# Kernel tuning notes

Measured on AMD Instinct MI355X. Metric: run time of the kernel, lower is better.

## Reference

```python
import jax, jax.numpy as jnp
import numpy as np

B, T, D = 8, 1024, 1024
H, G = 16, 4            # num_heads, query_groups
HD = D // H             # head_dim = 64
REP = H // G            # heads_per_group
EPS = 1e-10
NEG = -1e9


def setup_inputs() -> dict:
    key = jax.random.key(0)
    k1, k2, k3 = jax.random.split(key, 3)
    x = jax.random.normal(k1, (B, T, D), dtype=jnp.float32)
    w_qkv = jax.random.normal(k2, (D, H * HD + 2 * G * HD), dtype=jnp.float32) * (D ** -0.5)
    w_o = jax.random.normal(k3, (D, D), dtype=jnp.float32) * (D ** -0.5)
    padding_mask = jnp.ones((B, T), dtype=bool)
    return {"x": x, "w_qkv": w_qkv, "w_o": w_o, "padding_mask": padding_mask}


def _l2_norm(t):
    # qk_norm_type=2: L2 normalize over head_dim
    return t / (jnp.sqrt(jnp.sum(t * t, axis=-1, keepdims=True)) + EPS)


def reference(x, w_qkv, w_o, padding_mask):
    # fused QKV projection: [B,T,D] @ [D, H*HD + 2*G*HD]
    qkv = x @ w_qkv
    q, k, v = jnp.split(qkv, [H * HD, H * HD + G * HD], axis=-1)
    q = q.reshape(B, T, H, HD)
    k = k.reshape(B, T, G, HD)
    v = v.reshape(B, T, G, HD)
    # QK normalization (L2 over head_dim)
    q = _l2_norm(q)
    k = _l2_norm(k)
    # GQA: expand KV heads (repeat_interleave along head dim)
    k = jnp.repeat(k, REP, axis=2)  # [B,T,H,HD]
    v = jnp.repeat(v, REP, axis=2)
    # to [B,H,T,HD]
    q = q.transpose(0, 2, 1, 3)
    k = k.transpose(0, 2, 1, 3)
    v = v.transpose(0, 2, 1, 3)
    # causal + padding mask, True = attend
    causal = jnp.tril(jnp.ones((T, T), dtype=bool))  # [T_q, T_k]
    valid = padding_mask[:, None, :, None] & padding_mask[:, None, None, :] & causal[None, None]
    scale = HD ** -0.5  # SDPA default scale
    scores = jnp.einsum('bhqd,bhkd->bhqk', q, k) * scale
    scores = jnp.where(valid, scores, NEG)
    attn = jax.nn.softmax(scores, axis=-1)
    out = jnp.einsum('bhqk,bhkd->bhqd', attn, v)  # [B,H,T,HD]
    out = out.transpose(0, 2, 1, 3).reshape(B, T, D)
    return out @ w_o
```

## Files before the change

### kernel.cpp

```cpp
#include <hip/hip_runtime.h>
#include <hip/hip_bf16.h>

typedef __attribute__((ext_vector_type(8))) short short8;
typedef __attribute__((ext_vector_type(4))) short short4v;
typedef __attribute__((ext_vector_type(4))) float f32x4;

#define B_ 8
#define T_ 1024
#define D_ 1024
#define H_ 16
#define G_ 4
#define HD_ 64
#define QKVW 1536

#define GLOAD16(gp, lp) __builtin_amdgcn_global_load_lds( \
    (const __attribute__((address_space(1))) void*)(gp),  \
    (__attribute__((address_space(3))) void*)(lp), 16, 0, 0)

__device__ __forceinline__ float exp2_fast(float x) {
    return __builtin_amdgcn_exp2f(x);
}

__device__ __forceinline__ short8 pack_bf16x8(float4 a, float4 b) {
    union { short8 s; __hip_bfloat16 h[8]; } u;
    u.h[0] = __float2bfloat16(a.x); u.h[1] = __float2bfloat16(a.y);
    u.h[2] = __float2bfloat16(a.z); u.h[3] = __float2bfloat16(a.w);
    u.h[4] = __float2bfloat16(b.x); u.h[5] = __float2bfloat16(b.y);
    u.h[6] = __float2bfloat16(b.z); u.h[7] = __float2bfloat16(b.w);
    return u.s;
}

__global__ __launch_bounds__(256) void cvt_transpose(
    const float* __restrict__ in, __hip_bfloat16* __restrict__ outT, int K, int N)
{
    __shared__ float tile[32][33];
    const int k0 = blockIdx.y * 32, n0 = blockIdx.x * 32;
    const int r = threadIdx.x >> 5, c = threadIdx.x & 31;
    #pragma unroll
    for (int i = 0; i < 4; ++i)
        tile[r + i * 8][c] = in[(size_t)(k0 + r + i * 8) * N + n0 + c];
    __syncthreads();
    #pragma unroll
    for (int i = 0; i < 4; ++i)
        outT[(size_t)(n0 + r + i * 8) * K + k0 + c] = __float2bfloat16(tile[c][r + i * 8]);
}

__global__ __launch_bounds__(256) void gemm_qkv(
    const float* __restrict__ Af,
    const __hip_bfloat16* __restrict__ Bt,
    __hip_bfloat16* __restrict__ qkv,
    __hip_bfloat16* __restrict__ vt)
{
    const int M = B_ * T_, K = D_;
    __shared__ __hip_bfloat16 As[2][128 * 32];
    __shared__ __hip_bfloat16 Bs[2][128 * 32];

    const int tid  = threadIdx.x;
    const int lane = tid & 63;
    const int wr   = (tid >> 6) >> 1;
    const int wc   = (tid >> 6) & 1;

    const int rpx = (M >> 7) >> 3;
    const int xcd = blockIdx.x & 7;
    const int lin = blockIdx.x >> 3;
    const int by  = xcd * rpx + (lin % rpx);
    const int bx  = lin / rpx;
    const int m0 = by * 128;
    const int n0 = bx * 128;

    f32x4 acc[4][4] = {};

    const int sr0 = tid >> 2;
    const int sr1 = 64 + sr0;
    const int slot  = (tid & 3) ^ ((tid >> 3) & 3);
    const int sc_ln = (tid & 3) * 8;
    const int sc_sw = slot * 8;
    const int ws0 = sr0 * 64 + slot * 16;
    const int ws1 = sr1 * 64 + slot * 16;

    const float* Ar0f = Af + (size_t)(m0 + sr0) * K + sc_ln;
    const float* Ar1f = Af + (size_t)(m0 + sr1) * K + sc_ln;
    const __hip_bfloat16* Br0 = Bt + (size_t)(n0 + sr0) * K + sc_sw;
    const __hip_bfloat16* Br1 = Bt + (size_t)(n0 + sr1) * K + sc_sw;

    const int fr = lane & 15;
    const int kb = (lane >> 4) * 16;
    const int swzg = ((fr >> 1) & 3) << 4;

    float4 a0a = *(const float4*)(Ar0f);
    float4 a0b = *(const float4*)(Ar0f + 4);
    float4 a1a = *(const float4*)(Ar1f);
    float4 a1b = *(const float4*)(Ar1f + 4);
    GLOAD16(Br0, (char*)&Bs[0][0] + tid * 16);
    GLOAD16(Br1, (char*)&Bs[0][0] + 4096 + tid * 16);
    *(short8*)((char*)&As[0][0] + ws0) = pack_bf16x8(a0a, a0b);
    *(short8*)((char*)&As[0][0] + ws1) = pack_bf16x8(a1a, a1b);
    __syncthreads();

    int cur = 0;
    for (int kk = 0; kk < K; kk += 32) {
        const int nxt = cur ^ 1;
        const bool more = (kk + 32 < K);
        if (more) {
            a0a = *(const float4*)(Ar0f + kk + 32);
            a0b = *(const float4*)(Ar0f + kk + 36);
            a1a = *(const float4*)(Ar1f + kk + 32);
            a1b = *(const float4*)(Ar1f + kk + 36);
            GLOAD16(Br0 + kk + 32, (char*)&Bs[nxt][0] + tid * 16);
            GLOAD16(Br1 + kk + 32, (char*)&Bs[nxt][0] + 4096 + tid * 16);
        }
        short8 a[4], b[4];
        #pragma unroll
        for (int m = 0; m < 4; ++m)
            a[m] = *(const short8*)((char*)&As[cur][0] +
                    (wr * 64 + m * 16 + fr) * 64 + (kb ^ swzg));
        #pragma unroll
        for (int n = 0; n < 4; ++n)
            b[n] = *(const short8*)((char*)&Bs[cur][0] +
                    (wc * 64 + n * 16 + fr) * 64 + (kb ^ swzg));
        #pragma unroll
        for (int m = 0; m < 4; ++m)
            #pragma unroll
            for (int n = 0; n < 4; ++n)
                acc[m][n] = __builtin_amdgcn_mfma_f32_16x16x32_bf16(a[m], b[n], acc[m][n], 0, 0, 0);
        if (more) {
            *(short8*)((char*)&As[nxt][0] + ws0) = pack_bf16x8(a0a, a0b);
            *(short8*)((char*)&As[nxt][0] + ws1) = pack_bf16x8(a1a, a1b);
        }
        __syncthreads();
        cur = nxt;
    }

    const int rowb  = m0 + wr * 64 + (lane >> 4) * 4;
    const int colb0 = n0 + wc * 64;

    if (n0 < 1280) {
        const float extra = (n0 < 1024) ? 0.18033688f : 1.0f;
        #pragma unroll
        for (int m = 0; m < 4; ++m)
            #pragma unroll
            for (int r = 0; r < 4; ++r) {
                float ss = 0.f;
                #pragma unroll
                for (int n = 0; n < 4; ++n) { float v = acc[m][n][r]; ss += v * v; }
                ss += __shfl_xor(ss, 1, 64);
                ss += __shfl_xor(ss, 2, 64);
                ss += __shfl_xor(ss, 4, 64);
                ss += __shfl_xor(ss, 8, 64);
                float sc = extra / (sqrtf(ss) + 1e-10f);
                const size_t rbase = (size_t)(rowb + m * 16 + r) * QKVW + colb0 + fr;
                #pragma unroll
                for (int n = 0; n < 4; ++n)
                    qkv[rbase + n * 16] = __float2bfloat16(acc[m][n][r] * sc);
            }
    } else {
        #pragma unroll
        for (int m = 0; m < 4; ++m) {
            const int row = rowb + m * 16;
            const int bb  = row >> 10;
            const int t0  = row & 1023;
            #pragma unroll
            for (int n = 0; n < 4; ++n) {
                const int cv = colb0 + fr + n * 16 - 1280;
                const int gg = cv >> 6, d = cv & 63;
                union { short4v s; __hip_bfloat16 h[4]; } u;
                u.h[0] = __float2bfloat16(acc[m][n][0]);
                u.h[1] = __float2bfloat16(acc[m][n][1]);
                u.h[2] = __float2bfloat16(acc[m][n][2]);
                u.h[3] = __float2bfloat16(acc[m][n][3]);
                *reinterpret_cast<short4v*>(
                    vt + ((size_t)((bb * G_ + gg) * HD_ + d)) * T_ + t0) = u.s;
            }
        }
    }
}

__global__ __launch_bounds__(256) void gemm_tn_f32(
    const __hip_bfloat16* __restrict__ A,
    const __hip_bfloat16* __restrict__ Bt,
    float* __restrict__ C, int M, int N, int K)
{
    __shared__ __hip_bfloat16 As[2][128 * 32];
    __shared__ __hip_bfloat16 Bs[2][128 * 32];

    const int tid  = threadIdx.x;
    const int lane = tid & 63;
    const int wr   = (tid >> 6) >> 1;
    const int wc   = (tid >> 6) & 1;

    const int rpx = (M >> 7) >> 3;
    const int xcd = blockIdx.x & 7;
    const int lin = blockIdx.x >> 3;
    const int by  = xcd * rpx + (lin % rpx);
    const int bx  = lin / rpx;
    const int m0 = by * 128;
    const int n0 = bx * 128;

    f32x4 acc[4][4] = {};

    const int sr0 = tid >> 2;
    const int sr1 = 64 + sr0;
    const int slot  = (tid & 3) ^ ((tid >> 3) & 3);
    const int sc_sw = slot * 8;

    const __hip_bfloat16* Ar0 = A  + (size_t)(m0 + sr0) * K + sc_sw;
    const __hip_bfloat16* Ar1 = A  + (size_t)(m0 + sr1) * K + sc_sw;
    const __hip_bfloat16* Br0 = Bt + (size_t)(n0 + sr0) * K + sc_sw;
    const __hip_bfloat16* Br1 = Bt + (size_t)(n0 + sr1) * K + sc_sw;

    const int fr = lane & 15;
    const int kb = (lane >> 4) * 16;
    const int swzg = ((fr >> 1) & 3) << 4;

    GLOAD16(Ar0, (char*)&As[0][0] + tid * 16);
    GLOAD16(Ar1, (char*)&As[0][0] + 4096 + tid * 16);
    GLOAD16(Br0, (char*)&Bs[0][0] + tid * 16);
    GLOAD16(Br1, (char*)&Bs[0][0] + 4096 + tid * 16);
    __syncthreads();

    int cur = 0;
    for (int kk = 0; kk < K; kk += 32) {
        const int nxt = cur ^ 1;
        if (kk + 32 < K) {
            GLOAD16(Ar0 + kk + 32, (char*)&As[nxt][0] + tid * 16);
            GLOAD16(Ar1 + kk + 32, (char*)&As[nxt][0] + 4096 + tid * 16);
            GLOAD16(Br0 + kk + 32, (char*)&Bs[nxt][0] + tid * 16);
            GLOAD16(Br1 + kk + 32, (char*)&Bs[nxt][0] + 4096 + tid * 16);
        }
        short8 a[4], b[4];
        #pragma unroll
        for (int m = 0; m < 4; ++m)
            a[m] = *(const short8*)((char*)&As[cur][0] +
                    (wr * 64 + m * 16 + fr) * 64 + (kb ^ swzg));
        #pragma unroll
        for (int n = 0; n < 4; ++n)
            b[n] = *(const short8*)((char*)&Bs[cur][0] +
                    (wc * 64 + n * 16 + fr) * 64 + (kb ^ swzg));
        #pragma unroll
        for (int m = 0; m < 4; ++m)
            #pragma unroll
            for (int n = 0; n < 4; ++n)
                acc[m][n] = __builtin_amdgcn_mfma_f32_16x16x32_bf16(a[m], b[n], acc[m][n], 0, 0, 0);
        __syncthreads();
        cur = nxt;
    }

    const int rowb = m0 + wr * 64 + (lane >> 4) * 4;
    const int colb = n0 + wc * 64 + fr;
    #pragma unroll
    for (int m = 0; m < 4; ++m)
        #pragma unroll
        for (int n = 0; n < 4; ++n)
            #pragma unroll
            for (int r = 0; r < 4; ++r)
                C[(size_t)(rowb + m * 16 + r) * N + colb + n * 16] = acc[m][n][r];
}

__global__ __launch_bounds__(256) void attn_fwd(
    const __hip_bfloat16* __restrict__ qkv,
    const __hip_bfloat16* __restrict__ vt,
    __hip_bfloat16* __restrict__ out)
{
    const int pair = blockIdx.x;
    const int h  = blockIdx.y;
    const int b  = blockIdx.z;
    const int g  = h >> 2;

    const int tid  = threadIdx.x;
    const int lane = tid & 63;
    const int wid  = tid >> 6;

    __shared__ __hip_bfloat16 Ks[2 * 4096];
    __shared__ __hip_bfloat16 Vs[2 * 4096];
    __shared__ __hip_bfloat16 Ps[4 * 2048];

    const int fr  = lane & 15;
    const int kf  = (lane >> 4) * 8;
    const int kb  = kf * 2;
    const int swz = (fr & 7) << 4;

    const int srow = tid >> 3;
    const int scol = ((tid & 7) * 8) ^ ((srow & 7) << 3);

    const size_t kgbase = (size_t)(b * T_) * QKVW + H_ * HD_ + g * HD_ + scol;
    const size_t vgbase = (size_t)((b * G_ + g) * HD_) * T_ + scol;

    char* PsB = (char*)Ps + wid * 4096;

    auto stage = [&](int kt, int sl) {
        GLOAD16(qkv + kgbase + (size_t)(kt * 64 + srow) * QKVW,
                (char*)Ks + sl * 8192 + tid * 16);
        GLOAD16(qkv + kgbase + (size_t)(kt * 64 + 32 + srow) * QKVW,
                (char*)Ks + sl * 8192 + 4096 + tid * 16);
        GLOAD16(vt + vgbase + (size_t)srow * T_ + kt * 64,
                (char*)Vs + sl * 8192 + tid * 16);
        GLOAD16(vt + vgbase + (size_t)(32 + srow) * T_ + kt * 64,
                (char*)Vs + sl * 8192 + 4096 + tid * 16);
    };

    for (int half = 0; half < 2; ++half) {
        const int qt  = half ? (7 - pair) : pair;
        const int q0  = qt * 128;
        const int nkt = 2 * qt + 2;

        short8 qf[2][2];
        #pragma unroll
        for (int m = 0; m < 2; ++m) {
            const size_t qbase =
                ((size_t)(b * T_ + q0 + wid * 32 + m * 16 + fr)) * QKVW + h * HD_;
            qf[m][0] = *(const short8*)(qkv + qbase + kf);
            qf[m][1] = *(const short8*)(qkv + qbase + 32 + kf);
        }
        const int rb0 = q0 + wid * 32 + (lane >> 4) * 4;

        float lsum[2][4] = {};
        f32x4 o[2][4] = {};

        for (int kt = 0; kt < nkt; kt += 2) {
            stage(kt, 0);
            stage(kt + 1, 1);
            __syncthreads();

            #pragma unroll
            for (int sl = 0; sl < 2; ++sl) {
                const int  ck  = kt + sl;
                const bool msk = (ck >= nkt - 2);
                char* KsB = (char*)Ks + sl * 8192;
                char* VsB = (char*)Vs + sl * 8192;

                short8 bk0[4], bk1[4];
                #pragma unroll
                for (int nf = 0; nf < 4; ++nf) {
                    const int row = fr + 16 * nf;
                    bk0[nf] = *(const short8*)(KsB + row * 128 + (kb ^ swz));
                    bk1[nf] = *(const short8*)(KsB + row * 128 + ((64 + kb) ^ swz));
                }

                #pragma unroll
                for (int m = 0; m < 2; ++m) {
                    f32x4 s[4] = {};
                    __builtin_amdgcn_s_setprio(1);
                    #pragma unroll
                    for (int nf = 0; nf < 4; ++nf) {
                        s[nf] = __builtin_amdgcn_mfma_f32_16x16x32_bf16(qf[m][0], bk0[nf], s[nf], 0, 0, 0);
                        s[nf] = __builtin_amdgcn_mfma_f32_16x16x32_bf16(qf[m][1], bk1[nf], s[nf], 0, 0, 0);
                    }
                    __builtin_amdgcn_s_setprio(0);

                    if (msk) {
                        #pragma unroll
                        for (int nf = 0; nf < 4; ++nf) {
                            int col = ck * 64 + fr + 16 * nf;
                            #pragma unroll
                            for (int r = 0; r < 4; ++r) {
                                float p = (col <= rb0 + m * 16 + r) ? exp2_fast(s[nf][r]) : 0.f;
                                lsum[m][r] += p;
                                int q = m * 16 + (lane >> 4) * 4 + r;
                                *(__hip_bfloat16*)(PsB + q * 128 +
                                    ((2 * (fr + 16 * nf)) ^ ((q & 7) << 4))) = __float2bfloat16(p);
                            }
                        }
                    } else {
                        #pragma unroll
                        for (int nf = 0; nf < 4; ++nf)
                            #pragma unroll
                            for (int r = 0; r < 4; ++r) {
                                float p = exp2_fast(s[nf][r]);
                                lsum[m][r] += p;
                                int q = m * 16 + (lane >> 4) * 4 + r;
                                *(__hip_bfloat16*)(PsB + q * 128 +
                                    ((2 * (fr + 16 * nf)) ^ ((q & 7) << 4))) = __float2bfloat16(p);
                            }
                    }
                }

                short8 bv0[4], bv1[4];
                #pragma unroll
                for (int nf = 0; nf < 4; ++nf) {
                    const int row = fr + 16 * nf;
                    bv0[nf] = *(const short8*)(VsB + row * 128 + (kb ^ swz));
                    bv1[nf] = *(const short8*)(VsB + row * 128 + ((64 + kb) ^ swz));
                }
                __builtin_amdgcn_s_setprio(1);
                #pragma unroll
                for (int m = 0; m < 2; ++m) {
                    short8 pa0 = *(const short8*)(PsB + (m * 16 + fr) * 128 + (kb ^ swz));
                    short8 pa1 = *(const short8*)(PsB + (m * 16 + fr) * 128 + ((64 + kb) ^ swz));
                    #pragma unroll
                    for (int nf = 0; nf < 4; ++nf) {
                        o[m][nf] = __builtin_amdgcn_mfma_f32_16x16x32_bf16(pa0, bv0[nf], o[m][nf], 0, 0, 0);
                        o[m][nf] = __builtin_amdgcn_mfma_f32_16x16x32_bf16(pa1, bv1[nf], o[m][nf], 0, 0, 0);
                    }
                }
                __builtin_amdgcn_s_setprio(0);
            }
            __syncthreads();
        }

        #pragma unroll
        for (int m = 0; m < 2; ++m) {
            float linv[4];
            #pragma unroll
            for (int r = 0; r < 4; ++r) {
                float v = lsum[m][r];
                v += __shfl_xor(v, 1, 64);
                v += __shfl_xor(v, 2, 64);
                v += __shfl_xor(v, 4, 64);
                v += __shfl_xor(v, 8, 64);
                linv[r] = 1.0f / v;
            }
            #pragma unroll
            for (int nf = 0; nf < 4; ++nf) {
                int col = fr + 16 * nf;
                #pragma unroll
                for (int r = 0; r < 4; ++r) {
                    float v = o[m][nf][r] * linv[r];
                    out[((size_t)(b * T_ + rb0 + m * 16 + r)) * (H_ * HD_) + h * HD_ + col] =
                        __float2bfloat16(v);
                }
            }
        }
    }
}

extern "C" void kernel_launch(void* const* d_in, const int* in_sizes, int n_in,
                              void* d_out, int out_size, void* d_ws, size_t ws_size,
                              hipStream_t stream) {
    const float* x_f     = (const float*)d_in[0];
    const float* w_qkv_f = (const float*)d_in[1];
    const float* w_o_f   = (const float*)d_in[2];
    float* out = (float*)d_out;

    const int NX  = B_ * T_ * D_;
    const int NWQ = D_ * QKVW;
    const int NWO = D_ * D_;

    __hip_bfloat16* attn_out = (__hip_bfloat16*)d_ws;
    __hip_bfloat16* wqkvT = attn_out + NX;
    __hip_bfloat16* woT   = wqkvT + NWQ;
    __hip_bfloat16* qkv   = woT + NWO;
    __hip_bfloat16* vt    = qkv + (size_t)(B_ * T_) * QKVW;

    dim3 blk(256);

    cvt_transpose<<<dim3(QKVW / 32, D_ / 32), blk, 0, stream>>>(w_qkv_f, wqkvT, D_, QKVW);
    cvt_transpose<<<dim3(D_ / 32, D_ / 32), blk, 0, stream>>>(w_o_f, woT, D_, D_);

    gemm_qkv<<<dim3((QKVW / 128) * ((B_ * T_) / 128)), blk, 0, stream>>>(
        x_f, wqkvT, qkv, vt);

    attn_fwd<<<dim3(4, H_, B_), blk, 0, stream>>>(qkv, vt, attn_out);

    gemm_tn_f32<<<dim3((D_ / 128) * ((B_ * T_) / 128)), blk, 0, stream>>>(
        attn_out, woT, out, B_ * T_, D_, D_);
}
```

Measured before the change: 115.0 us.

## Triple-buffer GEMM shared tiles with explicit vmcnt waits and raw barriers

Both GEMM kernels move from double to triple buffering in shared memory, issuing global-to-LDS loads two k-steps ahead. The loop is fully unrolled over a fixed 32 k-steps, and __syncthreads is replaced by explicit s_waitcnt vmcnt/lgkmcnt counts plus s_barrier, so later loads can stay in flight across the barrier. The aim is to hide global memory latency behind MFMA work. The cost is more LDS per block (48KB), which may reduce occupancy. The hand-counted wait values are fragile, and KSTEPS hardcodes K=1024 in the generic gemm_tn_f32.

```diff
diff --git a/kernel.cpp b/kernel.cpp
--- a/kernel.cpp
+++ b/kernel.cpp
@@ -12,6 +12,7 @@
 #define G_ 4
 #define HD_ 64
 #define QKVW 1536
+#define KSTEPS 32
 
 #define GLOAD16(gp, lp) __builtin_amdgcn_global_load_lds( \
     (const __attribute__((address_space(1))) void*)(gp),  \
@@ -52,8 +53,8 @@
     __hip_bfloat16* __restrict__ vt)
 {
     const int M = B_ * T_, K = D_;
-    __shared__ __hip_bfloat16 As[2][128 * 32];
-    __shared__ __hip_bfloat16 Bs[2][128 * 32];
+    __shared__ __hip_bfloat16 As[3][128 * 32];
+    __shared__ __hip_bfloat16 Bs[3][128 * 32];
 
     const int tid  = threadIdx.x;
     const int lane = tid & 63;
@@ -87,48 +88,60 @@
     const int kb = (lane >> 4) * 16;
     const int swzg = ((fr >> 1) & 3) << 4;
 
-    float4 a0a = *(const float4*)(Ar0f);
-    float4 a0b = *(const float4*)(Ar0f + 4);
-    float4 a1a = *(const float4*)(Ar1f);
-    float4 a1b = *(const float4*)(Ar1f + 4);
-    GLOAD16(Br0, (char*)&Bs[0][0] + tid * 16);
-    GLOAD16(Br1, (char*)&Bs[0][0] + 4096 + tid * 16);
-    *(short8*)((char*)&As[0][0] + ws0) = pack_bf16x8(a0a, a0b);
-    *(short8*)((char*)&As[0][0] + ws1) = pack_bf16x8(a1a, a1b);
-    __syncthreads();
-
-    int cur = 0;
-    for (int kk = 0; kk < K; kk += 32) {
-        const int nxt = cur ^ 1;
-        const bool more = (kk + 32 < K);
-        if (more) {
-            a0a = *(const float4*)(Ar0f + kk + 32);
-            a0b = *(const float4*)(Ar0f + kk + 36);
-            a1a = *(const float4*)(Ar1f + kk + 32);
-            a1b = *(const float4*)(Ar1f + kk + 36);
-            GLOAD16(Br0 + kk + 32, (char*)&Bs[nxt][0] + tid * 16);
-            GLOAD16(Br1 + kk + 32, (char*)&Bs[nxt][0] + 4096 + tid * 16);
-        }
+    float4 ra[2][4];
+
+    auto stageB = [&](int t) {
+        GLOAD16(Br0 + t * 32, (char*)&Bs[t % 3][0] + tid * 16);
+        GLOAD16(Br1 + t * 32, (char*)&Bs[t % 3][0] + 4096 + tid * 16);
+    };
+    auto loadA = [&](int t) {
+        ra[t & 1][0] = *(const float4*)(Ar0f + t * 32);
+        ra[t & 1][1] = *(const float4*)(Ar0f + t * 32 + 4);
+        ra[t & 1][2] = *(const float4*)(Ar1f + t * 32);
+        ra[t & 1][3] = *(const float4*)(Ar1f + t * 32 + 4);
+    };
+    auto writeA = [&](int t) {
+        *(short8*)((char*)&As[t % 3][0] + ws0) = pack_bf16x8(ra[t & 1][0], ra[t & 1][1]);
+        *(short8*)((char*)&As[t % 3][0] + ws1) = pack_bf16x8(ra[t & 1][2], ra[t & 1][3]);
+    };
+
+    stageB(0); loadA(0);
+    stageB(1); loadA(1);
+    writeA(0);
+    asm volatile("s_waitcnt lgkmcnt(0)" ::: "memory");
+    asm volatile("s_waitcnt vmcnt(6)" ::: "memory");
+    __builtin_amdgcn_s_barrier();
+    __builtin_amdgcn_sched_barrier(0);
+
+    #pragma unroll
+    for (int t = 0; t < KSTEPS; ++t) {
+        if (t + 2 < KSTEPS) { stageB(t + 2); loadA(t + 2); }
+
         short8 a[4], b[4];
         #pragma unroll
         for (int m = 0; m < 4; ++m)
-            a[m] = *(const short8*)((char*)&As[cur][0] +
+            a[m] = *(const short8*)((char*)&As[t % 3][0] +
                     (wr * 64 + m * 16 + fr) * 64 + (kb ^ swzg));
         #pragma unroll
         for (int n = 0; n < 4; ++n)
-            b[n] = *(const short8*)((char*)&Bs[cur][0] +
+            b[n] = *(const short8*)((char*)&Bs[t % 3][0] +
                     (wc * 64 + n * 16 + fr) * 64 + (kb ^ swzg));
         #pragma unroll
         for (int m = 0; m < 4; ++m)
             #pragma unroll
             for (int n = 0; n < 4; ++n)
                 acc[m][n] = __builtin_amdgcn_mfma_f32_16x16x32_bf16(a[m], b[n], acc[m][n], 0, 0, 0);
-        if (more) {
-            *(short8*)((char*)&As[nxt][0] + ws0) = pack_bf16x8(a0a, a0b);
-            *(short8*)((char*)&As[nxt][0] + ws1) = pack_bf16x8(a1a, a1b);
-        }
-        __syncthreads();
-        cur = nxt;
+
+        if (t + 1 < KSTEPS) {
+            writeA(t + 1);
+            asm volatile("s_waitcnt lgkmcnt(0)" ::: "memory");
+            if (t + 2 < KSTEPS)
+                asm volatile("s_waitcnt vmcnt(6)" ::: "memory");
+            else
+                asm volatile("s_waitcnt vmcnt(0)" ::: "memory");
+            __builtin_amdgcn_s_barrier();
+            __builtin_amdgcn_sched_barrier(0);
+        }
     }
 
     const int rowb  = m0 + wr * 64 + (lane >> 4) * 4;
@@ -180,8 +193,8 @@
     const __hip_bfloat16* __restrict__ Bt,
     float* __restrict__ C, int M, int N, int K)
 {
-    __shared__ __hip_bfloat16 As[2][128 * 32];
-    __shared__ __hip_bfloat16 Bs[2][128 * 32];
+    __shared__ __hip_bfloat16 As[3][128 * 32];
+    __shared__ __hip_bfloat16 Bs[3][128 * 32];
 
     const int tid  = threadIdx.x;
     const int lane = tid & 63;
@@ -212,37 +225,46 @@
     const int kb = (lane >> 4) * 16;
     const int swzg = ((fr >> 1) & 3) << 4;
 
-    GLOAD16(Ar0, (char*)&As[0][0] + tid * 16);
-    GLOAD16(Ar1, (char*)&As[0][0] + 4096 + tid * 16);
-    GLOAD16(Br0, (char*)&Bs[0][0] + tid * 16);
-    GLOAD16(Br1, (char*)&Bs[0][0] + 4096 + tid * 16);
-    __syncthreads();
-
-    int cur = 0;
-    for (int kk = 0; kk < K; kk += 32) {
-        const int nxt = cur ^ 1;
-        if (kk + 32 < K) {
-            GLOAD16(Ar0 + kk + 32, (char*)&As[nxt][0] + tid * 16);
-            GLOAD16(Ar1 + kk + 32, (char*)&As[nxt][0] + 4096 + tid * 16);
-            GLOAD16(Br0 + kk + 32, (char*)&Bs[nxt][0] + tid * 16);
-            GLOAD16(Br1 + kk + 32, (char*)&Bs[nxt][0] + 4096 + tid * 16);
-        }
+    auto stage = [&](int t) {
+        GLOAD16(Ar0 + t * 32, (char*)&As[t % 3][0] + tid * 16);
+        GLOAD16(Ar1 + t * 32, (char*)&As[t % 3][0] + 4096 + tid * 16);
+        GLOAD16(Br0 + t * 32, (char*)&Bs[t % 3][0] + tid * 16);
+        GLOAD16(Br1 + t * 32, (char*)&Bs[t % 3][0] + 4096 + tid * 16);
+    };
+
+    stage(0);
+    stage(1);
+    asm volatile("s_waitcnt vmcnt(4)" ::: "memory");
+    __builtin_amdgcn_s_barrier();
+    __builtin_amdgcn_sched_barrier(0);
+
+    #pragma unroll
+    for (int t = 0; t < KSTEPS; ++t) {
+        if (t + 2 < KSTEPS) stage(t + 2);
+
         short8 a[4], b[4];
         #pragma unroll
         for (int m = 0; m < 4; ++m)
-            a[m] = *(const short8*)((char*)&As[cur][0] +
+            a[m] = *(const short8*)((char*)&As[t % 3][0] +
                     (wr * 64 + m * 16 + fr) * 64 + (kb ^ swzg));
         #pragma unroll
         for (int n = 0; n < 4; ++n)
-            b[n] = *(const short8*)((char*)&Bs[cur][0] +
+            b[n] = *(const short8*)((char*)&Bs[t % 3][0] +
                     (wc * 64 + n * 16 + fr) * 64 + (kb ^ swzg));
         #pragma unroll
         for (int m = 0; m < 4; ++m)
             #pragma unroll
             for (int n = 0; n < 4; ++n)
                 acc[m][n] = __builtin_amdgcn_mfma_f32_16x16x32_bf16(a[m], b[n], acc[m][n], 0, 0, 0);
-        __syncthreads();
-        cur = nxt;
+
+        if (t + 1 < KSTEPS) {
+            if (t + 2 < KSTEPS)
+                asm volatile("s_waitcnt vmcnt(4)" ::: "memory");
+            else
+                asm volatile("s_waitcnt vmcnt(0)" ::: "memory");
+            __builtin_amdgcn_s_barrier();
+            __builtin_amdgcn_sched_barrier(0);
+        }
     }
 
     const int rowb = m0 + wr * 64 + (lane >> 4) * 4;
```

After: 116.5 us. No clear change (+1.4%).
